# Kernel tuning notes

Hardware: AMD Instinct MI355X
Metric: run time of the kernel (lower is better)

## Reference

```python
import jax, jax.numpy as jnp
import numpy as np

N_NODES = 100000
N_EDGES = 1600000
F_IN = 128
HIDDEN = 64
N_CLASSES = 32


def setup_inputs() -> dict:
    key = jax.random.key(0)
    k1, k2, k3, k4 = jax.random.split(key, 4)
    x = jax.random.normal(k1, (N_NODES, F_IN), dtype=jnp.float32)
    edge_index = jax.random.randint(k2, (2, N_EDGES), 0, N_NODES, dtype=jnp.int32)
    # Glorot-style init for the two GCNConv weight matrices
    W1 = jax.random.normal(k3, (F_IN, HIDDEN), dtype=jnp.float32) * (1.0 / np.sqrt(F_IN))
    W2 = jax.random.normal(k4, (HIDDEN, N_CLASSES), dtype=jnp.float32) * (1.0 / np.sqrt(HIDDEN))
    b1 = jnp.zeros((HIDDEN,), dtype=jnp.float32)
    b2 = jnp.zeros((N_CLASSES,), dtype=jnp.float32)
    return {"x": x, "edge_index": edge_index, "W1": W1, "b1": b1, "W2": W2, "b2": b2}


def gcn_conv(x, W, b, src, dst, num_nodes):
    # PyG GCNConv: linear transform first, then normalized neighbor aggregation.
    h = x @ W  # [N, out]
    ones = jnp.ones(src.shape, dtype=h.dtype)
    deg = jax.ops.segment_sum(ones, dst, num_segments=num_nodes)  # in-degree incl. self-loops
    d_inv_sqrt = jnp.where(deg > 0, jax.lax.rsqrt(deg), 0.0)
    norm = d_inv_sqrt[src] * d_inv_sqrt[dst]  # [E]
    msg = h[src] * norm[:, None]              # gather + scale, [E, out]
    out = jax.ops.segment_sum(msg, dst, num_segments=num_nodes)  # scatter-add
    return out + b


def reference(x, edge_index, W1, b1, W2, b2):
    n = x.shape[0]
    # add_self_loops=True (GCNConv default)
    loop = jnp.arange(n, dtype=edge_index.dtype)
    src = jnp.concatenate([edge_index[0], loop])
    dst = jnp.concatenate([edge_index[1], loop])
    h = jax.nn.relu(gcn_conv(x, W1, b1, src, dst, n))
    # F.dropout(training=self.training) is identity in eval mode
    logits = gcn_conv(h, W2, b2, src, dst, n)
    return jax.nn.log_softmax(logits, axis=1)
```

## Files before the change

### kernel.cpp

```cpp
#include <hip/hip_runtime.h>

#define F_IN 128
#define HID 64
#define CLS 32
#define BCAP 4096

typedef short v8s __attribute__((ext_vector_type(8)));
typedef float f4 __attribute__((ext_vector_type(4)));
typedef float f2 __attribute__((ext_vector_type(2)));

__device__ __forceinline__ float bflo(unsigned int w) { return __uint_as_float(w << 16); }
__device__ __forceinline__ float bfhi(unsigned int w) { return __uint_as_float(w & 0xFFFF0000u); }
__device__ __forceinline__ unsigned short f2bf(float f) {
    unsigned int u = __float_as_uint(f);
    u += 0x7FFFu + ((u >> 16) & 1u);
    return (unsigned short)(u >> 16);
}
__device__ __forceinline__ unsigned int pack2(float lo, float hi) {
    unsigned int r;
    asm("v_cvt_pk_bf16_f32 %0, %1, %2" : "=v"(r) : "v"(lo), "v"(hi));
    return r;
}
__device__ __forceinline__ unsigned char f2fp8(float v) {
    return (unsigned char)(__builtin_amdgcn_cvt_pk_fp8_f32(v, v, 0, false) & 0xFF);
}

__global__ __launch_bounds__(256) void k_front(const int* __restrict__ src,
                                               const int* __restrict__ dst,
                                               int* __restrict__ bC,
                                               int* __restrict__ bucketed,
                                               const float* __restrict__ x,
                                               const float* __restrict__ W1,
                                               unsigned char* __restrict__ y,
                                               int E, int nb, int n, int sB) {
    __shared__ union {
        struct { int h[1024]; int chunk[1024]; } sc;
        unsigned short w1[HID * 136];
    } S;
    int tid = threadIdx.x;
    int bid = blockIdx.x;

    if (bid < sB) {
        for (int i = tid; i < nb; i += 256) S.sc.h[i] = 0;
        __syncthreads();
        int e0 = bid << 12;
        int myRec[16], myB[16], myRank[16];
#pragma unroll
        for (int k = 0; k < 16; ++k) {
            int e = e0 + k * 256 + tid;
            if (e < E) {
                int d = dst[e];
                myB[k] = d >> 7;
                myRec[k] = src[e] | ((d & 127) << 17);
                myRank[k] = atomicAdd(&S.sc.h[myB[k]], 1);
            } else {
                myB[k] = -1;
            }
        }
        __syncthreads();
        for (int i = tid; i < nb; i += 256)
            S.sc.chunk[i] = S.sc.h[i] ? (i * BCAP + atomicAdd(&bC[i], S.sc.h[i])) : 0;
        __syncthreads();
#pragma unroll
        for (int k = 0; k < 16; ++k)
            if (myB[k] >= 0) bucketed[S.sc.chunk[myB[k]] + myRank[k]] = myRec[k];
    } else {
        for (int i = tid; i < F_IN * HID; i += 256) {
            int k = i >> 6, nn = i & 63;
            S.w1[nn * 136 + k] = f2bf(W1[i]);
        }
        __syncthreads();
        int lane = tid & 63;
        int quad = lane >> 4, c = lane & 15;
        int nstripes = (n + 15) >> 4;
        int stripe = (bid - sB) * 4 + (tid >> 6);
        if (stripe >= nstripes) return;
        int row0 = stripe << 4;

        f4 acc[4] = {};
        union { unsigned int u[4]; v8s v; } au;
#pragma unroll
        for (int ks = 0; ks < 4; ++ks) {
            int k0 = ks * 32 + quad * 8;
            int row = row0 + c;
            if (row >= n) row = n - 1;
            const float* xp = x + (size_t)row * F_IN + k0;
            float4 lo = *(const float4*)xp;
            float4 hi = *(const float4*)(xp + 4);
            au.u[0] = pack2(lo.x, lo.y);
            au.u[1] = pack2(lo.z, lo.w);
            au.u[2] = pack2(hi.x, hi.y);
            au.u[3] = pack2(hi.z, hi.w);
            v8s a = au.v;
#pragma unroll
            for (int nt = 0; nt < 4; ++nt) {
                v8s bb = *(const v8s*)&S.w1[(nt * 16 + c) * 136 + k0];
                acc[nt] = __builtin_amdgcn_mfma_f32_16x16x32_bf16(a, bb, acc[nt], 0, 0, 0);
            }
        }
#pragma unroll
        for (int reg = 0; reg < 4; ++reg) {
            int row = row0 + quad * 4 + reg;
            if (row < n) {
#pragma unroll
                for (int nt = 0; nt < 4; ++nt)
                    y[(size_t)row * HID + nt * 16 + c] = f2fp8(acc[nt][reg]);
            }
        }
    }
}

__global__ __launch_bounds__(512) void k_csr(const int* __restrict__ bC,
                                             const int* __restrict__ bucketed,
                                             int* __restrict__ pk,
                                             float* __restrict__ dinv, int* __restrict__ csr,
                                             int n) {
    __shared__ int cnt[128];
    __shared__ int s[128];
    __shared__ int baseS[128];
    int b = blockIdx.x;
    int node0 = b << 7;
    int tid = threadIdx.x;
    if (tid < 128) cnt[tid] = 0;
    __syncthreads();
    int nrec = bC[b];
    if (nrec > BCAP) nrec = BCAP;
    int p0 = b * BCAP, p1 = p0 + nrec;

    int rec[8], rnk[8];
#pragma unroll
    for (int k = 0; k < 8; ++k) {
        int p = p0 + tid + (k << 9);
        if (p < p1) {
            int r = bucketed[p];
            rec[k] = r;
            rnk[k] = atomicAdd(&cnt[r >> 17], 1);
        } else {
            rec[k] = -1;
        }
    }
    __syncthreads();
    int v = 0, pv = 0;
    if (tid < 128) { v = cnt[tid]; pv = (v + 3) & ~3; s[tid] = pv; }
    __syncthreads();
    for (int off = 1; off < 128; off <<= 1) {
        int t = (tid >= off && tid < 128) ? s[tid - off] : 0;
        __syncthreads();
        if (tid < 128) s[tid] += t;
        __syncthreads();
    }
    if (tid < 128) {
        int myoff = p0 + s[tid] - pv;
        baseS[tid] = myoff;
        int node = node0 + tid;
        if (node < n) {
            pk[node] = myoff | (v << 22);
            dinv[node] = rsqrtf((float)(v + 1));
        }
    }
    __syncthreads();
#pragma unroll
    for (int k = 0; k < 8; ++k) {
        if (rec[k] >= 0) csr[baseS[rec[k] >> 17] + rnk[k]] = rec[k] & 0x1FFFF;
    }
}

__global__ __launch_bounds__(256) void k_gather64_w2(const int* __restrict__ pk,
                                                     const int* __restrict__ csr,
                                                     const unsigned char* __restrict__ xw8,
                                                     const float* __restrict__ b1,
                                                     const float* __restrict__ W2,
                                                     const float* __restrict__ dinv,
                                                     unsigned short* __restrict__ y2, int n) {
    __shared__ unsigned short Wt[CLS * 72];
    __shared__ unsigned short Hl[32 * 72];
    int tid = threadIdx.x;
    for (int i = tid; i < HID * CLS; i += 256) {
        int k = i >> 5, nn = i & 31;
        Wt[nn * 72 + k] = f2bf(W2[i]);
    }

    int g = tid >> 3;
    int l = tid & 7;
    int node = blockIdx.x * 32 + g;

    if (node < n) {
        unsigned int pv = (unsigned int)pk[node];
        int p0 = pv & 0x3FFFFF;
        int cntv = (int)(pv >> 22);
        int p1 = p0 + cntv;
        float dd = dinv[node];
        uint2 sw = *(const uint2*)(xw8 + (size_t)node * HID + l * 8);

        f2 a0 = {0.f, 0.f}, a1 = a0, a2 = a0, a3 = a0;
        f2 c0 = a0, c1 = a0, c2 = a0, c3 = a0;
        int q = p0;
        for (; q + 3 < p1; q += 4) {
            int4 ss = *(const int4*)(csr + q);
            float d0 = dinv[ss.x], d1 = dinv[ss.y], d2 = dinv[ss.z], d3 = dinv[ss.w];
            uint2 w0 = *(const uint2*)(xw8 + (size_t)ss.x * HID + l * 8);
            uint2 w1 = *(const uint2*)(xw8 + (size_t)ss.y * HID + l * 8);
            uint2 w2 = *(const uint2*)(xw8 + (size_t)ss.z * HID + l * 8);
            uint2 w3 = *(const uint2*)(xw8 + (size_t)ss.w * HID + l * 8);
            f2 D0 = {d0, d0}, D1 = {d1, d1}, D2 = {d2, d2}, D3 = {d3, d3};
            a0 += __builtin_amdgcn_cvt_pk_f32_fp8(w0.x, false) * D0;
            a1 += __builtin_amdgcn_cvt_pk_f32_fp8(w0.x, true) * D0;
            a2 += __builtin_amdgcn_cvt_pk_f32_fp8(w0.y, false) * D0;
            a3 += __builtin_amdgcn_cvt_pk_f32_fp8(w0.y, true) * D0;
            c0 += __builtin_amdgcn_cvt_pk_f32_fp8(w1.x, false) * D1;
            c1 += __builtin_amdgcn_cvt_pk_f32_fp8(w1.x, true) * D1;
            c2 += __builtin_amdgcn_cvt_pk_f32_fp8(w1.y, false) * D1;
            c3 += __builtin_amdgcn_cvt_pk_f32_fp8(w1.y, true) * D1;
            a0 += __builtin_amdgcn_cvt_pk_f32_fp8(w2.x, false) * D2;
            a1 += __builtin_amdgcn_cvt_pk_f32_fp8(w2.x, true) * D2;
            a2 += __builtin_amdgcn_cvt_pk_f32_fp8(w2.y, false) * D2;
            a3 += __builtin_amdgcn_cvt_pk_f32_fp8(w2.y, true) * D2;
            c0 += __builtin_amdgcn_cvt_pk_f32_fp8(w3.x, false) * D3;
            c1 += __builtin_amdgcn_cvt_pk_f32_fp8(w3.x, true) * D3;
            c2 += __builtin_amdgcn_cvt_pk_f32_fp8(w3.y, false) * D3;
            c3 += __builtin_amdgcn_cvt_pk_f32_fp8(w3.y, true) * D3;
        }
        for (; q < p1; ++q) {
            int s0 = csr[q];
            float d0 = dinv[s0];
            uint2 w0 = *(const uint2*)(xw8 + (size_t)s0 * HID + l * 8);
            f2 D0 = {d0, d0};
            a0 += __builtin_amdgcn_cvt_pk_f32_fp8(w0.x, false) * D0;
            a1 += __builtin_amdgcn_cvt_pk_f32_fp8(w0.x, true) * D0;
            a2 += __builtin_amdgcn_cvt_pk_f32_fp8(w0.y, false) * D0;
            a3 += __builtin_amdgcn_cvt_pk_f32_fp8(w0.y, true) * D0;
        }
        a0 += c0; a1 += c1; a2 += c2; a3 += c3;
        f2 DS = {dd, dd};
        a0 += __builtin_amdgcn_cvt_pk_f32_fp8(sw.x, false) * DS;
        a1 += __builtin_amdgcn_cvt_pk_f32_fp8(sw.x, true) * DS;
        a2 += __builtin_amdgcn_cvt_pk_f32_fp8(sw.y, false) * DS;
        a3 += __builtin_amdgcn_cvt_pk_f32_fp8(sw.y, true) * DS;

        float4 bb0 = *(const float4*)(b1 + l * 8);
        float4 bb1 = *(const float4*)(b1 + l * 8 + 4);
        float h0 = fmaxf(a0.x * dd + bb0.x, 0.f);
        float h1 = fmaxf(a0.y * dd + bb0.y, 0.f);
        float h2 = fmaxf(a1.x * dd + bb0.z, 0.f);
        float h3 = fmaxf(a1.y * dd + bb0.w, 0.f);
        float h4 = fmaxf(a2.x * dd + bb1.x, 0.f);
        float h5 = fmaxf(a2.y * dd + bb1.y, 0.f);
        float h6 = fmaxf(a3.x * dd + bb1.z, 0.f);
        float h7 = fmaxf(a3.y * dd + bb1.w, 0.f);
        uint4 hp;
        hp.x = pack2(h0, h1);
        hp.y = pack2(h2, h3);
        hp.z = pack2(h4, h5);
        hp.w = pack2(h6, h7);
        *(uint4*)&Hl[g * 72 + l * 8] = hp;
    }
    __syncthreads();

    int wv = tid >> 6;
    int t = wv & 1, nt = wv >> 1;
    int lane = tid & 63, quad = lane >> 4, c = lane & 15;
    f4 acc = {};
#pragma unroll
    for (int ks = 0; ks < 2; ++ks) {
        int k0 = ks * 32 + quad * 8;
        v8s aF = *(const v8s*)&Hl[(t * 16 + c) * 72 + k0];
        v8s bF = *(const v8s*)&Wt[(nt * 16 + c) * 72 + k0];
        acc = __builtin_amdgcn_mfma_f32_16x16x32_bf16(aF, bF, acc, 0, 0, 0);
    }
    int row0 = blockIdx.x * 32 + t * 16;
#pragma unroll
    for (int reg = 0; reg < 4; ++reg) {
        int row = row0 + quad * 4 + reg;
        if (row < n) {
            float dd2 = dinv[row];
            y2[(size_t)row * CLS + nt * 16 + c] = f2bf(acc[reg] * dd2);
        }
    }
}

__global__ __launch_bounds__(256) void k_gather32_lsm(const int* __restrict__ pk,
                                                      const int* __restrict__ csr,
                                                      const unsigned short* __restrict__ hwb,
                                                      const float* __restrict__ b,
                                                      const float* __restrict__ dinv,
                                                      float* __restrict__ out, int n) {
    int tid = threadIdx.x;
    int node = blockIdx.x * 64 + (tid >> 2);
    if (node >= n) return;
    int l = tid & 3;
    unsigned int pv = (unsigned int)pk[node];
    int p0 = pv & 0x3FFFFF;
    int cntv = (int)(pv >> 22);
    int p1 = p0 + cntv;
    float dd = dinv[node];
    uint4 sw = *(const uint4*)(hwb + (size_t)node * CLS + l * 8);

    float A0 = 0.f, A1 = 0.f, A2 = 0.f, A3 = 0.f, A4 = 0.f, A5 = 0.f, A6 = 0.f, A7 = 0.f;
    float B0 = 0.f, B1 = 0.f, B2 = 0.f, B3 = 0.f, B4 = 0.f, B5 = 0.f, B6 = 0.f, B7 = 0.f;
    int p = p0;
    for (; p + 3 < p1; p += 4) {
        int4 ss = *(const int4*)(csr + p);
        uint4 w0 = *(const uint4*)(hwb + (size_t)ss.x * CLS + l * 8);
        uint4 w1 = *(const uint4*)(hwb + (size_t)ss.y * CLS + l * 8);
        uint4 w2 = *(const uint4*)(hwb + (size_t)ss.z * CLS + l * 8);
        uint4 w3 = *(const uint4*)(hwb + (size_t)ss.w * CLS + l * 8);
        A0 += bflo(w0.x); A1 += bfhi(w0.x); A2 += bflo(w0.y); A3 += bfhi(w0.y);
        A4 += bflo(w0.z); A5 += bfhi(w0.z); A6 += bflo(w0.w); A7 += bfhi(w0.w);
        B0 += bflo(w1.x); B1 += bfhi(w1.x); B2 += bflo(w1.y); B3 += bfhi(w1.y);
        B4 += bflo(w1.z); B5 += bfhi(w1.z); B6 += bflo(w1.w); B7 += bfhi(w1.w);
        A0 += bflo(w2.x); A1 += bfhi(w2.x); A2 += bflo(w2.y); A3 += bfhi(w2.y);
        A4 += bflo(w2.z); A5 += bfhi(w2.z); A6 += bflo(w2.w); A7 += bfhi(w2.w);
        B0 += bflo(w3.x); B1 += bfhi(w3.x); B2 += bflo(w3.y); B3 += bfhi(w3.y);
        B4 += bflo(w3.z); B5 += bfhi(w3.z); B6 += bflo(w3.w); B7 += bfhi(w3.w);
    }
    for (; p < p1; ++p) {
        int s0 = csr[p];
        uint4 w0 = *(const uint4*)(hwb + (size_t)s0 * CLS + l * 8);
        A0 += bflo(w0.x); A1 += bfhi(w0.x); A2 += bflo(w0.y); A3 += bfhi(w0.y);
        A4 += bflo(w0.z); A5 += bfhi(w0.z); A6 += bflo(w0.w); A7 += bfhi(w0.w);
    }
    A0 += B0; A1 += B1; A2 += B2; A3 += B3;
    A4 += B4; A5 += B5; A6 += B6; A7 += B7;

    float4 bb0 = *(const float4*)(b + l * 8);
    float4 bb1 = *(const float4*)(b + l * 8 + 4);
    float v0 = (A0 + bflo(sw.x)) * dd + bb0.x;
    float v1 = (A1 + bfhi(sw.x)) * dd + bb0.y;
    float v2 = (A2 + bflo(sw.y)) * dd + bb0.z;
    float v3 = (A3 + bfhi(sw.y)) * dd + bb0.w;
    float v4 = (A4 + bflo(sw.z)) * dd + bb1.x;
    float v5 = (A5 + bfhi(sw.z)) * dd + bb1.y;
    float v6 = (A6 + bflo(sw.w)) * dd + bb1.z;
    float v7 = (A7 + bfhi(sw.w)) * dd + bb1.w;

    float m = fmaxf(fmaxf(fmaxf(v0, v1), fmaxf(v2, v3)), fmaxf(fmaxf(v4, v5), fmaxf(v6, v7)));
    m = fmaxf(m, __shfl_xor(m, 1));
    m = fmaxf(m, __shfl_xor(m, 2));
    float s = __expf(v0 - m) + __expf(v1 - m) + __expf(v2 - m) + __expf(v3 - m) +
              __expf(v4 - m) + __expf(v5 - m) + __expf(v6 - m) + __expf(v7 - m);
    s += __shfl_xor(s, 1);
    s += __shfl_xor(s, 2);
    float ls = m + __logf(s);
    float4 o0, o1;
    o0.x = v0 - ls; o0.y = v1 - ls; o0.z = v2 - ls; o0.w = v3 - ls;
    o1.x = v4 - ls; o1.y = v5 - ls; o1.z = v6 - ls; o1.w = v7 - ls;
    float* op = out + (size_t)node * CLS + l * 8;
    *(float4*)op = o0;
    *(float4*)(op + 4) = o1;
}

extern "C" void kernel_launch(void* const* d_in, const int* in_sizes, int n_in,
                              void* d_out, int out_size, void* d_ws, size_t ws_size,
                              hipStream_t stream) {
    const float* x  = (const float*)d_in[0];
    const int* edge = (const int*)d_in[1];
    const float* W1 = (const float*)d_in[2];
    const float* b1 = (const float*)d_in[3];
    const float* W2 = (const float*)d_in[4];
    const float* b2 = (const float*)d_in[5];
    float* out = (float*)d_out;

    int N = in_sizes[0] / F_IN;
    int E = in_sizes[1] / 2;
    const int* src = edge;
    const int* dst = edge + E;
    int NB = (N + 127) >> 7;

    float* dinv    = (float*)d_ws;
    int* pk        = (int*)(dinv + N);
    int* bC        = pk + N;
    int* csr       = bC + 1024;
    int* bucketed  = csr + (size_t)NB * BCAP;
    unsigned char* bufA = (unsigned char*)(bucketed + (size_t)NB * BCAP);
    unsigned short* y2  = (unsigned short*)(bufA + (size_t)N * HID);

    hipMemsetAsync(bC, 0, (size_t)NB * sizeof(int), stream);

    int sB = (E + 4095) / 4096;
    int nstripes16 = (N + 15) >> 4;
    int gB = (nstripes16 + 3) / 4;

    k_front<<<sB + gB, 256, 0, stream>>>(src, dst, bC, bucketed, x, W1, bufA, E, NB, N, sB);

    k_csr<<<NB, 512, 0, stream>>>(bC, bucketed, pk, dinv, csr, N);

    k_gather64_w2<<<(N + 31) / 32, 256, 0, stream>>>(pk, csr, bufA, b1, W2, dinv, y2, N);

    k_gather32_lsm<<<(N + 63) / 64, 256, 0, stream>>>(pk, csr, y2, b2, dinv, out, N);
}
```

Baseline: 193.0 us.

## Fuse CSR construction into gather kernels using per-bucket LDS adjacency lists

Removes the global CSR array and packed offsets. A light kernel now only counts degrees to produce dinv, and each gather kernel rebuilds its 128-node bucket's adjacency list in shared memory from the bucketed records. The 64-wide gather moves to 4 lanes per node with 16-byte loads and runs 128 nodes per block, with the W2 MFMA done per block. This avoids the global CSR write and read-back, at the cost of redoing the bucket sort twice, using 16KB+ of LDS per block, and launching fewer, larger blocks.

```diff
diff --git a/kernel.cpp b/kernel.cpp
--- a/kernel.cpp
+++ b/kernel.cpp
@@ -110,29 +110,53 @@
     }
 }
 
-__global__ __launch_bounds__(512) void k_csr(const int* __restrict__ bC,
+__global__ __launch_bounds__(256) void k_cnt(const int* __restrict__ bC,
                                              const int* __restrict__ bucketed,
-                                             int* __restrict__ pk,
-                                             float* __restrict__ dinv, int* __restrict__ csr,
-                                             int n) {
+                                             float* __restrict__ dinv, int n) {
     __shared__ int cnt[128];
-    __shared__ int s[128];
-    __shared__ int baseS[128];
-    int b = blockIdx.x;
-    int node0 = b << 7;
-    int tid = threadIdx.x;
+    int tid = threadIdx.x, b = blockIdx.x;
     if (tid < 128) cnt[tid] = 0;
     __syncthreads();
     int nrec = bC[b];
     if (nrec > BCAP) nrec = BCAP;
-    int p0 = b * BCAP, p1 = p0 + nrec;
-
+    int p0 = b * BCAP;
+    for (int p = tid; p < nrec; p += 256) atomicAdd(&cnt[bucketed[p0 + p] >> 17], 1);
+    __syncthreads();
+    if (tid < 128) {
+        int node = (b << 7) + tid;
+        if (node < n) dinv[node] = rsqrtf((float)(cnt[tid] + 1));
+    }
+}
+
+__global__ __launch_bounds__(512) void k_g64(const int* __restrict__ bC,
+                                             const int* __restrict__ bucketed,
+                                             const unsigned char* __restrict__ xw8,
+                                             const float* __restrict__ b1,
+                                             const float* __restrict__ W2,
+                                             const float* __restrict__ dinv,
+                                             unsigned short* __restrict__ y2, int n) {
+    __shared__ int lidx[BCAP];
+    __shared__ int cnt[128], sS[128], baseL[128];
+    __shared__ unsigned short Wt[CLS * 72];
+    __shared__ unsigned short Hl[128 * 72];
+    int tid = threadIdx.x, b = blockIdx.x;
+    int node0 = b << 7;
+
+    for (int i = tid; i < HID * CLS; i += 512) {
+        int k = i >> 5, nn = i & 31;
+        Wt[nn * 72 + k] = f2bf(W2[i]);
+    }
+    if (tid < 128) cnt[tid] = 0;
+    __syncthreads();
+    int nrec = bC[b];
+    if (nrec > BCAP) nrec = BCAP;
+    int p0 = b * BCAP;
     int rec[8], rnk[8];
 #pragma unroll
     for (int k = 0; k < 8; ++k) {
-        int p = p0 + tid + (k << 9);
-        if (p < p1) {
-            int r = bucketed[p];
+        int p = tid + (k << 9);
+        if (p < nrec) {
+            int r = bucketed[p0 + p];
             rec[k] = r;
             rnk[k] = atomicAdd(&cnt[r >> 17], 1);
         } else {
@@ -140,190 +164,198 @@
         }
     }
     __syncthreads();
-    int v = 0, pv = 0;
-    if (tid < 128) { v = cnt[tid]; pv = (v + 3) & ~3; s[tid] = pv; }
+    int v = 0;
+    if (tid < 128) { v = cnt[tid]; sS[tid] = v; }
     __syncthreads();
     for (int off = 1; off < 128; off <<= 1) {
-        int t = (tid >= off && tid < 128) ? s[tid - off] : 0;
-        __syncthreads();
-        if (tid < 128) s[tid] += t;
-        __syncthreads();
-    }
-    if (tid < 128) {
-        int myoff = p0 + s[tid] - pv;
-        baseS[tid] = myoff;
-        int node = node0 + tid;
-        if (node < n) {
-            pk[node] = myoff | (v << 22);
-            dinv[node] = rsqrtf((float)(v + 1));
-        }
-    }
-    __syncthreads();
-#pragma unroll
-    for (int k = 0; k < 8; ++k) {
-        if (rec[k] >= 0) csr[baseS[rec[k] >> 17] + rnk[k]] = rec[k] & 0x1FFFF;
-    }
-}
-
-__global__ __launch_bounds__(256) void k_gather64_w2(const int* __restrict__ pk,
-                                                     const int* __restrict__ csr,
-                                                     const unsigned char* __restrict__ xw8,
-                                                     const float* __restrict__ b1,
-                                                     const float* __restrict__ W2,
-                                                     const float* __restrict__ dinv,
-                                                     unsigned short* __restrict__ y2, int n) {
-    __shared__ unsigned short Wt[CLS * 72];
-    __shared__ unsigned short Hl[32 * 72];
-    int tid = threadIdx.x;
-    for (int i = tid; i < HID * CLS; i += 256) {
-        int k = i >> 5, nn = i & 31;
-        Wt[nn * 72 + k] = f2bf(W2[i]);
-    }
-
-    int g = tid >> 3;
-    int l = tid & 7;
-    int node = blockIdx.x * 32 + g;
-
+        int t = (tid >= off && tid < 128) ? sS[tid - off] : 0;
+        __syncthreads();
+        if (tid < 128) sS[tid] += t;
+        __syncthreads();
+    }
+    if (tid < 128) baseL[tid] = sS[tid] - v;
+    __syncthreads();
+#pragma unroll
+    for (int k = 0; k < 8; ++k)
+        if (rec[k] >= 0) lidx[baseL[rec[k] >> 17] + rnk[k]] = rec[k] & 0x1FFFF;
+    __syncthreads();
+
+    int g = tid >> 2, l = tid & 3;
+    int node = node0 + g;
     if (node < n) {
-        unsigned int pv = (unsigned int)pk[node];
-        int p0 = pv & 0x3FFFFF;
-        int cntv = (int)(pv >> 22);
-        int p1 = p0 + cntv;
-        float dd = dinv[node];
-        uint2 sw = *(const uint2*)(xw8 + (size_t)node * HID + l * 8);
-
-        f2 a0 = {0.f, 0.f}, a1 = a0, a2 = a0, a3 = a0;
-        f2 c0 = a0, c1 = a0, c2 = a0, c3 = a0;
-        int q = p0;
-        for (; q + 3 < p1; q += 4) {
-            int4 ss = *(const int4*)(csr + q);
-            float d0 = dinv[ss.x], d1 = dinv[ss.y], d2 = dinv[ss.z], d3 = dinv[ss.w];
-            uint2 w0 = *(const uint2*)(xw8 + (size_t)ss.x * HID + l * 8);
-            uint2 w1 = *(const uint2*)(xw8 + (size_t)ss.y * HID + l * 8);
-            uint2 w2 = *(const uint2*)(xw8 + (size_t)ss.z * HID + l * 8);
-            uint2 w3 = *(const uint2*)(xw8 + (size_t)ss.w * HID + l * 8);
-            f2 D0 = {d0, d0}, D1 = {d1, d1}, D2 = {d2, d2}, D3 = {d3, d3};
+        int cv = cnt[g];
+        float dd = rsqrtf((float)(cv + 1));
+        int q = baseL[g], q1 = baseL[g] + cv;
+        uint4 sw = *(const uint4*)(xw8 + (size_t)node * HID + l * 16);
+
+        f2 a0 = {0.f, 0.f}, a1 = a0, a2 = a0, a3 = a0, a4 = a0, a5 = a0, a6 = a0, a7 = a0;
+        f2 c0 = a0, c1 = a0, c2 = a0, c3 = a0, c4 = a0, c5 = a0, c6 = a0, c7 = a0;
+        for (; q + 1 < q1; q += 2) {
+            int s0 = lidx[q], s1 = lidx[q + 1];
+            float dv0 = dinv[s0], dv1 = dinv[s1];
+            uint4 w0 = *(const uint4*)(xw8 + (size_t)s0 * HID + l * 16);
+            uint4 w1 = *(const uint4*)(xw8 + (size_t)s1 * HID + l * 16);
+            f2 D0 = {dv0, dv0}, D1 = {dv1, dv1};
             a0 += __builtin_amdgcn_cvt_pk_f32_fp8(w0.x, false) * D0;
             a1 += __builtin_amdgcn_cvt_pk_f32_fp8(w0.x, true) * D0;
             a2 += __builtin_amdgcn_cvt_pk_f32_fp8(w0.y, false) * D0;
             a3 += __builtin_amdgcn_cvt_pk_f32_fp8(w0.y, true) * D0;
+            a4 += __builtin_amdgcn_cvt_pk_f32_fp8(w0.z, false) * D0;
+            a5 += __builtin_amdgcn_cvt_pk_f32_fp8(w0.z, true) * D0;
+            a6 += __builtin_amdgcn_cvt_pk_f32_fp8(w0.w, false) * D0;
+            a7 += __builtin_amdgcn_cvt_pk_f32_fp8(w0.w, true) * D0;
             c0 += __builtin_amdgcn_cvt_pk_f32_fp8(w1.x, false) * D1;
             c1 += __builtin_amdgcn_cvt_pk_f32_fp8(w1.x, true) * D1;
             c2 += __builtin_amdgcn_cvt_pk_f32_fp8(w1.y, false) * D1;
             c3 += __builtin_amdgcn_cvt_pk_f32_fp8(w1.y, true) * D1;
-            a0 += __builtin_amdgcn_cvt_pk_f32_fp8(w2.x, false) * D2;
-            a1 += __builtin_amdgcn_cvt_pk_f32_fp8(w2.x, true) * D2;
-            a2 += __builtin_amdgcn_cvt_pk_f32_fp8(w2.y, false) * D2;
-            a3 += __builtin_amdgcn_cvt_pk_f32_fp8(w2.y, true) * D2;
-            c0 += __builtin_amdgcn_cvt_pk_f32_fp8(w3.x, false) * D3;
-            c1 += __builtin_amdgcn_cvt_pk_f32_fp8(w3.x, true) * D3;
-            c2 += __builtin_amdgcn_cvt_pk_f32_fp8(w3.y, false) * D3;
-            c3 += __builtin_amdgcn_cvt_pk_f32_fp8(w3.y, true) * D3;
-        }
-        for (; q < p1; ++q) {
-            int s0 = csr[q];
-            float d0 = dinv[s0];
-            uint2 w0 = *(const uint2*)(xw8 + (size_t)s0 * HID + l * 8);
-            f2 D0 = {d0, d0};
+            c4 += __builtin_amdgcn_cvt_pk_f32_fp8(w1.z, false) * D1;
+            c5 += __builtin_amdgcn_cvt_pk_f32_fp8(w1.z, true) * D1;
+            c6 += __builtin_amdgcn_cvt_pk_f32_fp8(w1.w, false) * D1;
+            c7 += __builtin_amdgcn_cvt_pk_f32_fp8(w1.w, true) * D1;
+        }
+        if (q < q1) {
+            int s0 = lidx[q];
+            float dv0 = dinv[s0];
+            uint4 w0 = *(const uint4*)(xw8 + (size_t)s0 * HID + l * 16);
+            f2 D0 = {dv0, dv0};
             a0 += __builtin_amdgcn_cvt_pk_f32_fp8(w0.x, false) * D0;
             a1 += __builtin_amdgcn_cvt_pk_f32_fp8(w0.x, true) * D0;
             a2 += __builtin_amdgcn_cvt_pk_f32_fp8(w0.y, false) * D0;
             a3 += __builtin_amdgcn_cvt_pk_f32_fp8(w0.y, true) * D0;
+            a4 += __builtin_amdgcn_cvt_pk_f32_fp8(w0.z, false) * D0;
+            a5 += __builtin_amdgcn_cvt_pk_f32_fp8(w0.z, true) * D0;
+            a6 += __builtin_amdgcn_cvt_pk_f32_fp8(w0.w, false) * D0;
+            a7 += __builtin_amdgcn_cvt_pk_f32_fp8(w0.w, true) * D0;
         }
         a0 += c0; a1 += c1; a2 += c2; a3 += c3;
+        a4 += c4; a5 += c5; a6 += c6; a7 += c7;
         f2 DS = {dd, dd};
         a0 += __builtin_amdgcn_cvt_pk_f32_fp8(sw.x, false) * DS;
         a1 += __builtin_amdgcn_cvt_pk_f32_fp8(sw.x, true) * DS;
         a2 += __builtin_amdgcn_cvt_pk_f32_fp8(sw.y, false) * DS;
         a3 += __builtin_amdgcn_cvt_pk_f32_fp8(sw.y, true) * DS;
-
-        float4 bb0 = *(const float4*)(b1 + l * 8);
-        float4 bb1 = *(const float4*)(b1 + l * 8 + 4);
-        float h0 = fmaxf(a0.x * dd + bb0.x, 0.f);
-        float h1 = fmaxf(a0.y * dd + bb0.y, 0.f);
-        float h2 = fmaxf(a1.x * dd + bb0.z, 0.f);
-        float h3 = fmaxf(a1.y * dd + bb0.w, 0.f);
-        float h4 = fmaxf(a2.x * dd + bb1.x, 0.f);
-        float h5 = fmaxf(a2.y * dd + bb1.y, 0.f);
-        float h6 = fmaxf(a3.x * dd + bb1.z, 0.f);
-        float h7 = fmaxf(a3.y * dd + bb1.w, 0.f);
-        uint4 hp;
-        hp.x = pack2(h0, h1);
-        hp.y = pack2(h2, h3);
-        hp.z = pack2(h4, h5);
-        hp.w = pack2(h6, h7);
-        *(uint4*)&Hl[g * 72 + l * 8] = hp;
-    }
-    __syncthreads();
-
-    int wv = tid >> 6;
-    int t = wv & 1, nt = wv >> 1;
-    int lane = tid & 63, quad = lane >> 4, c = lane & 15;
-    f4 acc = {};
-#pragma unroll
-    for (int ks = 0; ks < 2; ++ks) {
-        int k0 = ks * 32 + quad * 8;
-        v8s aF = *(const v8s*)&Hl[(t * 16 + c) * 72 + k0];
-        v8s bF = *(const v8s*)&Wt[(nt * 16 + c) * 72 + k0];
-        acc = __builtin_amdgcn_mfma_f32_16x16x32_bf16(aF, bF, acc, 0, 0, 0);
-    }
-    int row0 = blockIdx.x * 32 + t * 16;
-#pragma unroll
-    for (int reg = 0; reg < 4; ++reg) {
-        int row = row0 + quad * 4 + reg;
-        if (row < n) {
-            float dd2 = dinv[row];
-            y2[(size_t)row * CLS + nt * 16 + c] = f2bf(acc[reg] * dd2);
-        }
-    }
-}
-
-__global__ __launch_bounds__(256) void k_gather32_lsm(const int* __restrict__ pk,
-                                                      const int* __restrict__ csr,
-                                                      const unsigned short* __restrict__ hwb,
-                                                      const float* __restrict__ b,
-                                                      const float* __restrict__ dinv,
-                                                      float* __restrict__ out, int n) {
-    int tid = threadIdx.x;
-    int node = blockIdx.x * 64 + (tid >> 2);
+        a4 += __builtin_amdgcn_cvt_pk_f32_fp8(sw.z, false) * DS;
+        a5 += __builtin_amdgcn_cvt_pk_f32_fp8(sw.z, true) * DS;
+        a6 += __builtin_amdgcn_cvt_pk_f32_fp8(sw.w, false) * DS;
+        a7 += __builtin_amdgcn_cvt_pk_f32_fp8(sw.w, true) * DS;
+
+        float4 bb0 = *(const float4*)(b1 + l * 16);
+        float4 bb1 = *(const float4*)(b1 + l * 16 + 4);
+        float4 bb2 = *(const float4*)(b1 + l * 16 + 8);
+        float4 bb3 = *(const float4*)(b1 + l * 16 + 12);
+        float h0  = fmaxf(a0.x * dd + bb0.x, 0.f), h1  = fmaxf(a0.y * dd + bb0.y, 0.f);
+        float h2  = fmaxf(a1.x * dd + bb0.z, 0.f), h3  = fmaxf(a1.y * dd + bb0.w, 0.f);
+        float h4  = fmaxf(a2.x * dd + bb1.x, 0.f), h5  = fmaxf(a2.y * dd + bb1.y, 0.f);
+        float h6  = fmaxf(a3.x * dd + bb1.z, 0.f), h7  = fmaxf(a3.y * dd + bb1.w, 0.f);
+        float h8  = fmaxf(a4.x * dd + bb2.x, 0.f), h9  = fmaxf(a4.y * dd + bb2.y, 0.f);
+        float h10 = fmaxf(a5.x * dd + bb2.z, 0.f), h11 = fmaxf(a5.y * dd + bb2.w, 0.f);
+        float h12 = fmaxf(a6.x * dd + bb3.x, 0.f), h13 = fmaxf(a6.y * dd + bb3.y, 0.f);
+        float h14 = fmaxf(a7.x * dd + bb3.z, 0.f), h15 = fmaxf(a7.y * dd + bb3.w, 0.f);
+        uint4* hbp = (uint4*)&Hl[g * 72 + l * 16];
+        hbp[0] = make_uint4(pack2(h0, h1), pack2(h2, h3), pack2(h4, h5), pack2(h6, h7));
+        hbp[1] = make_uint4(pack2(h8, h9), pack2(h10, h11), pack2(h12, h13), pack2(h14, h15));
+    }
+    __syncthreads();
+
+    int wv = tid >> 6, lane = tid & 63, quad = lane >> 4, c = lane & 15;
+    int ct = wv & 1;
+    int rt0 = wv >> 1;
+#pragma unroll
+    for (int rr = 0; rr < 2; ++rr) {
+        int rt = rt0 + rr * 4;
+        f4 acc = {};
+#pragma unroll
+        for (int ks = 0; ks < 2; ++ks) {
+            int k0 = ks * 32 + quad * 8;
+            v8s aF = *(const v8s*)&Hl[(rt * 16 + c) * 72 + k0];
+            v8s bF = *(const v8s*)&Wt[(ct * 16 + c) * 72 + k0];
+            acc = __builtin_amdgcn_mfma_f32_16x16x32_bf16(aF, bF, acc, 0, 0, 0);
+        }
+#pragma unroll
+        for (int reg = 0; reg < 4; ++reg) {
+            int rl = rt * 16 + quad * 4 + reg;
+            int row = node0 + rl;
+            if (row < n) {
+                float dd2 = rsqrtf((float)(cnt[rl] + 1));
+                y2[(size_t)row * CLS + ct * 16 + c] = f2bf(acc[reg] * dd2);
+            }
+        }
+    }
+}
+
+__global__ __launch_bounds__(512) void k_g32(const int* __restrict__ bC,
+                                             const int* __restrict__ bucketed,
+                                             const unsigned short* __restrict__ y2,
+                                             const float* __restrict__ b2,
+                                             float* __restrict__ out, int n) {
+    __shared__ int lidx[BCAP];
+    __shared__ int cnt[128], sS[128], baseL[128];
+    int tid = threadIdx.x, b = blockIdx.x;
+    int node0 = b << 7;
+    if (tid < 128) cnt[tid] = 0;
+    __syncthreads();
+    int nrec = bC[b];
+    if (nrec > BCAP) nrec = BCAP;
+    int p0 = b * BCAP;
+    int rec[8], rnk[8];
+#pragma unroll
+    for (int k = 0; k < 8; ++k) {
+        int p = tid + (k << 9);
+        if (p < nrec) {
+            int r = bucketed[p0 + p];
+            rec[k] = r;
+            rnk[k] = atomicAdd(&cnt[r >> 17], 1);
+        } else {
+            rec[k] = -1;
+        }
+    }
+    __syncthreads();
+    int v = 0;
+    if (tid < 128) { v = cnt[tid]; sS[tid] = v; }
+    __syncthreads();
+    for (int off = 1; off < 128; off <<= 1) {
+        int t = (tid >= off && tid < 128) ? sS[tid - off] : 0;
+        __syncthreads();
+        if (tid < 128) sS[tid] += t;
+        __syncthreads();
+    }
+    if (tid < 128) baseL[tid] = sS[tid] - v;
+    __syncthreads();
+#pragma unroll
+    for (int k = 0; k < 8; ++k)
+        if (rec[k] >= 0) lidx[baseL[rec[k] >> 17] + rnk[k]] = rec[k] & 0x1FFFF;
+    __syncthreads();
+
+    int g = tid >> 2, l = tid & 3;
+    int node = node0 + g;
     if (node >= n) return;
-    int l = tid & 3;
-    unsigned int pv = (unsigned int)pk[node];
-    int p0 = pv & 0x3FFFFF;
-    int cntv = (int)(pv >> 22);
-    int p1 = p0 + cntv;
-    float dd = dinv[node];
-    uint4 sw = *(const uint4*)(hwb + (size_t)node * CLS + l * 8);
+    int cv = cnt[g];
+    float dd = rsqrtf((float)(cv + 1));
+    int q = baseL[g], q1 = baseL[g] + cv;
+    uint4 sw = *(const uint4*)(y2 + (size_t)node * CLS + l * 8);
 
     float A0 = 0.f, A1 = 0.f, A2 = 0.f, A3 = 0.f, A4 = 0.f, A5 = 0.f, A6 = 0.f, A7 = 0.f;
     float B0 = 0.f, B1 = 0.f, B2 = 0.f, B3 = 0.f, B4 = 0.f, B5 = 0.f, B6 = 0.f, B7 = 0.f;
-    int p = p0;
-    for (; p + 3 < p1; p += 4) {
-        int4 ss = *(const int4*)(csr + p);
-        uint4 w0 = *(const uint4*)(hwb + (size_t)ss.x * CLS + l * 8);
-        uint4 w1 = *(const uint4*)(hwb + (size_t)ss.y * CLS + l * 8);
-        uint4 w2 = *(const uint4*)(hwb + (size_t)ss.z * CLS + l * 8);
-        uint4 w3 = *(const uint4*)(hwb + (size_t)ss.w * CLS + l * 8);
+    for (; q + 1 < q1; q += 2) {
+        int s0 = lidx[q], s1 = lidx[q + 1];
+        uint4 w0 = *(const uint4*)(y2 + (size_t)s0 * CLS + l * 8);
+        uint4 w1 = *(const uint4*)(y2 + (size_t)s1 * CLS + l * 8);
         A0 += bflo(w0.x); A1 += bfhi(w0.x); A2 += bflo(w0.y); A3 += bfhi(w0.y);
         A4 += bflo(w0.z); A5 += bfhi(w0.z); A6 += bflo(w0.w); A7 += bfhi(w0.w);
         B0 += bflo(w1.x); B1 += bfhi(w1.x); B2 += bflo(w1.y); B3 += bfhi(w1.y);
         B4 += bflo(w1.z); B5 += bfhi(w1.z); B6 += bflo(w1.w); B7 += bfhi(w1.w);
-        A0 += bflo(w2.x); A1 += bfhi(w2.x); A2 += bflo(w2.y); A3 += bfhi(w2.y);
-        A4 += bflo(w2.z); A5 += bfhi(w2.z); A6 += bflo(w2.w); A7 += bfhi(w2.w);
-        B0 += bflo(w3.x); B1 += bfhi(w3.x); B2 += bflo(w3.y); B3 += bfhi(w3.y);
-        B4 += bflo(w3.z); B5 += bfhi(w3.z); B6 += bflo(w3.w); B7 += bfhi(w3.w);
-    }
-    for (; p < p1; ++p) {
-        int s0 = csr[p];
-        uint4 w0 = *(const uint4*)(hwb + (size_t)s0 * CLS + l * 8);
+    }
+    if (q < q1) {
+        int s0 = lidx[q];
+        uint4 w0 = *(const uint4*)(y2 + (size_t)s0 * CLS + l * 8);
         A0 += bflo(w0.x); A1 += bfhi(w0.x); A2 += bflo(w0.y); A3 += bfhi(w0.y);
         A4 += bflo(w0.z); A5 += bfhi(w0.z); A6 += bflo(w0.w); A7 += bfhi(w0.w);
     }
     A0 += B0; A1 += B1; A2 += B2; A3 += B3;
     A4 += B4; A5 += B5; A6 += B6; A7 += B7;
 
-    float4 bb0 = *(const float4*)(b + l * 8);
-    float4 bb1 = *(const float4*)(b + l * 8 + 4);
+    float4 bb0 = *(const float4*)(b2 + l * 8);
+    float4 bb1 = *(const float4*)(b2 + l * 8 + 4);
     float v0 = (A0 + bflo(sw.x)) * dd + bb0.x;
     float v1 = (A1 + bfhi(sw.x)) * dd + bb0.y;
     float v2 = (A2 + bflo(sw.y)) * dd + bb0.z;
@@ -367,14 +399,12 @@
     int NB = (N + 127) >> 7;
 
     float* dinv    = (float*)d_ws;
-    int* pk        = (int*)(dinv + N);
-    int* bC        = pk + N;
-    int* csr       = bC + 1024;
-    int* bucketed  = csr + (size_t)NB * BCAP;
+    int* bC        = (int*)(dinv + N);
+    int* bucketed  = bC + 1024;
     unsigned char* bufA = (unsigned char*)(bucketed + (size_t)NB * BCAP);
     unsigned short* y2  = (unsigned short*)(bufA + (size_t)N * HID);
 
-    hipMemsetAsync(bC, 0, (size_t)NB * sizeof(int), stream);
+    (void)hipMemsetAsync(bC, 0, (size_t)NB * sizeof(int), stream);
 
     int sB = (E + 4095) / 4096;
     int nstripes16 = (N + 15) >> 4;
@@ -382,9 +412,9 @@
 
     k_front<<<sB + gB, 256, 0, stream>>>(src, dst, bC, bucketed, x, W1, bufA, E, NB, N, sB);
 
-    k_csr<<<NB, 512, 0, stream>>>(bC, bucketed, pk, dinv, csr, N);
-
-    k_gather64_w2<<<(N + 31) / 32, 256, 0, stream>>>(pk, csr, bufA, b1, W2, dinv, y2, N);
-
-    k_gather32_lsm<<<(N + 63) / 64, 256, 0, stream>>>(pk, csr, y2, b2, dinv, out, N);
-}
+    k_cnt<<<NB, 256, 0, stream>>>(bC, bucketed, dinv, N);
+
+    k_g64<<<NB, 512, 0, stream>>>(bC, bucketed, bufA, b1, W2, dinv, y2, N);
+
+    k_g32<<<NB, 512, 0, stream>>>(bC, bucketed, y2, b2, out, N);
+}
```

Result: faster. 187.6 us (-2.8%).
